# Kernel tuning notes

Measured on AMD Instinct MI355X. Metric: run time of the kernel, lower is better.

The kernel has to match this reference:

```python
import jax, jax.numpy as jnp
import numpy as np

EMBED_DIM = 1024
NUM_HEADS = 16
HEAD_DIM = EMBED_DIM // NUM_HEADS


def setup_inputs() -> dict:
    key = jax.random.key(0)
    k_x, k_wqkv, k_bqkv, k_wo, k_bo = jax.random.split(key, 5)
    B, T, C = 4, 2048, EMBED_DIM
    s_in = 1.0 / np.sqrt(C)
    return {
        "x": jax.random.normal(k_x, (B, T, C), dtype=jnp.float32),
        # torch Linear: weight [out,in]; we store transposed [in,out] for x @ W
        "w_qkv": jax.random.uniform(k_wqkv, (C, 3 * C), dtype=jnp.float32, minval=-s_in, maxval=s_in),
        "b_qkv": jax.random.uniform(k_bqkv, (3 * C,), dtype=jnp.float32, minval=-s_in, maxval=s_in),
        "w_out": jax.random.uniform(k_wo, (C, C), dtype=jnp.float32, minval=-s_in, maxval=s_in),
        "b_out": jax.random.uniform(k_bo, (C,), dtype=jnp.float32, minval=-s_in, maxval=s_in),
    }


def reference(x, w_qkv, b_qkv, w_out, b_out):
    B, T, C = x.shape
    H, D = NUM_HEADS, HEAD_DIM
    qkv = x @ w_qkv + b_qkv                       # [B,T,3C]
    qkv = qkv.reshape(B, T, 3, H, D)
    q, k, v = qkv[:, :, 0], qkv[:, :, 1], qkv[:, :, 2]   # [B,T,H,D]
    q = q.transpose(0, 2, 1, 3)                   # [B,H,T,D]
    k = k.transpose(0, 2, 1, 3)
    v = v.transpose(0, 2, 1, 3)
    scale = 1.0 / np.sqrt(D).astype(np.float32)
    att = jnp.einsum("bhqd,bhkd->bhqk", q, k) * scale   # [B,H,T,T]
    causal = jnp.tril(jnp.ones((T, T), dtype=bool))
    att = jnp.where(causal[None, None], att, -jnp.inf)
    att = jax.nn.softmax(att, axis=-1)
    y = jnp.einsum("bhqk,bhkd->bhqd", att, v)     # [B,H,T,D]
    y = y.transpose(0, 2, 1, 3).reshape(B, T, C)
    return y @ w_out + b_out
```

## Files before the change

### kernel.cpp

```cpp
#include <hip/hip_runtime.h>
#include <hip/hip_bf16.h>

#define EMBED 1024
#define NHEAD 16
#define HDIM  64
#define BATCH 4
#define SEQ   2048
#define BT    (BATCH*SEQ)
#define NQKV  (3*EMBED)

using bf16x8 = __attribute__((ext_vector_type(8))) short;
using f32x4  = __attribute__((ext_vector_type(4))) float;

__device__ __forceinline__ unsigned short f2bf(float f){
  union { float f; unsigned u; } v; v.f = f;
  unsigned r = v.u + 0x7FFFu + ((v.u >> 16) & 1u);
  return (unsigned short)(r >> 16);
}

__device__ __forceinline__ float exp2_hw(float x){
  float r; asm("v_exp_f32 %0, %1" : "=v"(r) : "v"(x)); return r;
}
__device__ __forceinline__ unsigned cvtpk_bf16(float lo, float hi){
  unsigned r; asm("v_cvt_pk_bf16_f32 %0, %1, %2" : "=v"(r) : "v"(lo), "v"(hi));
  return r;
}

__device__ __forceinline__ void gload_lds16(const void* g, void* l){
  __builtin_amdgcn_global_load_lds(
      (const __attribute__((address_space(1))) void*)g,
      (__attribute__((address_space(3))) void*)l, 16, 0, 0);
}

__global__ __launch_bounds__(256) void cvt_f32_bf16_k(
    const float* __restrict__ in, unsigned short* __restrict__ out, int n)
{
  int i = (blockIdx.x * 256 + threadIdx.x) * 4;
  if (i >= n) return;
  float4 v = *(const float4*)&in[i];
  ushort4 o;
  o.x = f2bf(v.x); o.y = f2bf(v.y); o.z = f2bf(v.z); o.w = f2bf(v.w);
  *(ushort4*)&out[i] = o;
}

__global__ __launch_bounds__(256) void transpose_cvt_k(
    const float* __restrict__ in, unsigned short* __restrict__ out, int R, int C)
{
  __shared__ float tile[32][33];
  int tx = threadIdx.x, ty = threadIdx.y;
  int c0 = blockIdx.x * 32, r0 = blockIdx.y * 32;
#pragma unroll
  for (int j = ty; j < 32; j += 8)
    tile[j][tx] = in[(size_t)(r0 + j) * C + c0 + tx];
  __syncthreads();
#pragma unroll
  for (int j = ty; j < 32; j += 8)
    out[(size_t)(c0 + j) * R + r0 + tx] = f2bf(tile[tx][j]);
}

template<int EPI>
__global__ __launch_bounds__(256) void gemm_bt(
    const unsigned short* __restrict__ A,
    const unsigned short* __restrict__ Bt,
    const float* __restrict__ bias,
    unsigned short* __restrict__ qp,
    unsigned short* __restrict__ kp,
    unsigned short* __restrict__ vp,
    float* __restrict__ outp,
    int M, int N, int K)
{
  __shared__ unsigned short As[2][128 * 32];
  __shared__ unsigned short Bs[2][128 * 32];
  const int tid = threadIdx.x;
  const int w = tid >> 6, lane = tid & 63;
  const int lr = lane & 15, lg = lane >> 4;
  const int gy = gridDim.y;
  const int lin = (int)(blockIdx.y * gridDim.x + blockIdx.x);
  const int cpx = (int)(gridDim.x * gy) >> 3;
  const int wg = (lin & 7) * cpx + (lin >> 3);
  const int m0 = (wg / gy) * 128, n0 = (wg % gy) * 128;
  const int wm = (w >> 1) * 64, wn = (w & 1) * 64;
  f32x4 acc[4][4] = {};

  int goff[2], dst[2];
#pragma unroll
  for (int i = 0; i < 2; i++) {
    int f = (w * 2 + i) * 512 + lane * 8;
    goff[i] = (f >> 5) * K + (f & 31);
    dst[i] = f;
  }
  const unsigned short* pA = A + (size_t)m0 * K;
  const unsigned short* pB = Bt + (size_t)n0 * K;

  const int nkt = K >> 5;

#pragma unroll
  for (int i = 0; i < 2; i++) {
    gload_lds16(pA + goff[i], &As[0][dst[i]]);
    gload_lds16(pB + goff[i], &Bs[0][dst[i]]);
  }

  int cur = 0;
  for (int t = 0; t < nkt; t++) {
    if (t + 1 < nkt) {
      const int kt = (t + 1) << 5;
#pragma unroll
      for (int i = 0; i < 2; i++) {
        gload_lds16(pA + goff[i] + kt, &As[cur ^ 1][dst[i]]);
        gload_lds16(pB + goff[i] + kt, &Bs[cur ^ 1][dst[i]]);
      }
      asm volatile("s_waitcnt vmcnt(4)" ::: "memory");
    } else {
      asm volatile("s_waitcnt vmcnt(0)" ::: "memory");
    }
    __builtin_amdgcn_s_barrier();
    __builtin_amdgcn_sched_barrier(0);

    bf16x8 af[4], bv[4];
#pragma unroll
    for (int mi = 0; mi < 4; mi++)
      af[mi] = *(const bf16x8*)&As[cur][(wm + mi * 16 + lr) * 32 + lg * 8];
#pragma unroll
    for (int ni = 0; ni < 4; ni++)
      bv[ni] = *(const bf16x8*)&Bs[cur][(wn + ni * 16 + lr) * 32 + lg * 8];
    __builtin_amdgcn_s_setprio(1);
#pragma unroll
    for (int mi = 0; mi < 4; mi++)
#pragma unroll
      for (int ni = 0; ni < 4; ni++)
        acc[mi][ni] = __builtin_amdgcn_mfma_f32_16x16x32_bf16(af[mi], bv[ni], acc[mi][ni], 0, 0, 0);
    __builtin_amdgcn_s_setprio(0);

    asm volatile("s_waitcnt lgkmcnt(0)" ::: "memory");
    __builtin_amdgcn_s_barrier();
    cur ^= 1;
  }

#pragma unroll
  for (int mi = 0; mi < 4; mi++)
#pragma unroll
    for (int ni = 0; ni < 4; ni++) {
      const int rowb = m0 + wm + mi * 16 + lg * 4;
      const int colb = n0 + wn + ni * 16 + lr;
      const float bv_ = bias[colb];
      if (EPI == 0) {
        int s = colb >> 10, hh = (colb & 1023) >> 6, d = colb & 63;
        int b = rowb >> 11, t = rowb & 2047;
        if (s == 2) {
          ushort4 o4;
          o4.x = f2bf(acc[mi][ni][0] + bv_);
          o4.y = f2bf(acc[mi][ni][1] + bv_);
          o4.z = f2bf(acc[mi][ni][2] + bv_);
          o4.w = f2bf(acc[mi][ni][3] + bv_);
          *(ushort4*)&vp[((size_t)(b * NHEAD + hh) * HDIM + d) * SEQ + t] = o4;
        } else {
          unsigned short* dst_ = (s == 0) ? qp : kp;
          const float scl = (s == 0) ? 0.18033688f : 1.0f;
#pragma unroll
          for (int r = 0; r < 4; r++)
            dst_[((size_t)(b * NHEAD + hh) * SEQ + t + r) * HDIM + d] =
                f2bf((acc[mi][ni][r] + bv_) * scl);
        }
      } else {
#pragma unroll
        for (int r = 0; r < 4; r++)
          outp[(size_t)(rowb + r) * N + colb] = acc[mi][ni][r] + bv_;
      }
    }
}

__device__ __forceinline__ void softmax_frag(
    f32x4 (&s)[4], float& m, f32x4& su, f32x4 (&o)[4],
    unsigned short* psrow, int qrow, int kbase, bool needmask,
    int lg, int lr, int pswz)
{
  const float NEG = -1e30f;
  if (needmask) {
#pragma unroll
    for (int n = 0; n < 4; n++)
#pragma unroll
      for (int r = 0; r < 4; r++) {
        if (kbase + n * 16 + lg * 4 + r > qrow) s[n][r] = NEG;
      }
  }
  float t0 = fmaxf(fmaxf(s[0][0], s[0][1]), fmaxf(s[0][2], s[0][3]));
  float t1 = fmaxf(fmaxf(s[1][0], s[1][1]), fmaxf(s[1][2], s[1][3]));
  float t2 = fmaxf(fmaxf(s[2][0], s[2][1]), fmaxf(s[2][2], s[2][3]));
  float t3 = fmaxf(fmaxf(s[3][0], s[3][1]), fmaxf(s[3][2], s[3][3]));
  float pm = fmaxf(fmaxf(t0, t1), fmaxf(t2, t3));
  if (__any(pm > m + 8.f)) {
    pm = fmaxf(pm, __shfl_xor(pm, 16, 64));
    pm = fmaxf(pm, __shfl_xor(pm, 32, 64));
    float mn = fmaxf(m, pm);
    float fac = exp2_hw(m - mn);
    m = mn;
    float fr[4];
#pragma unroll
    for (int r = 0; r < 4; r++) fr[r] = __shfl(fac, lg * 4 + r, 64);
#pragma unroll
    for (int r = 0; r < 4; r++) su[r] *= fr[r];
#pragma unroll
    for (int n = 0; n < 4; n++)
#pragma unroll
      for (int r = 0; r < 4; r++) o[n][r] *= fr[r];
  }
#pragma unroll
  for (int n = 0; n < 4; n++) {
    float p0 = exp2_hw(s[n][0] - m);
    float p1 = exp2_hw(s[n][1] - m);
    float p2 = exp2_hw(s[n][2] - m);
    float p3 = exp2_hw(s[n][3] - m);
    uint2 pk;
    pk.x = cvtpk_bf16(p0, p1);
    pk.y = cvtpk_bf16(p2, p3);
    int E = (lr * 64 + n * 16 + lg * 4) ^ pswz;
    *(uint2*)&psrow[E] = pk;
  }
}

__global__ __launch_bounds__(256) void attn_k(
    const unsigned short* __restrict__ Q,
    const unsigned short* __restrict__ K,
    const unsigned short* __restrict__ Vt,
    unsigned short* __restrict__ Y)
{
  __shared__ unsigned short Ks[2][64 * 64];
  __shared__ unsigned short Vs[2][64 * 64];
  __shared__ unsigned short Ps[4][32 * 64];

  const int tid = threadIdx.x;
  const int w = tid >> 6, lane = tid & 63;
  const int lr = lane & 15, lg = lane >> 4;
  const int bh = blockIdx.y;
  const int b = bh >> 4, h = bh & 15;
  const size_t base = (size_t)bh * SEQ * HDIM;
  const float NEG = -1e30f;
  const int pswz = (lr & 7) << 3;

  bf16x8 ones;
#pragma unroll
  for (int e = 0; e < 8; e++) ones[e] = (short)0x3F80;

  const int f0 = w * 128 + lane, f1 = f0 + 64;
  const int r0_ = f0 >> 3, c0_ = ((f0 & 7) ^ (r0_ & 7)) * 8;
  const int r1_ = f1 >> 3, c1_ = ((f1 & 7) ^ (r1_ & 7)) * 8;

  for (int seg = 0; seg < 2; seg++) {
    const int qb = seg ? (int)blockIdx.x : (15 - (int)blockIdx.x);
    const int qw0 = qb * 128 + w * 32;
    const int nk = 2 * qb + 2;

    bf16x8 aq[2][2];
#pragma unroll
    for (int f = 0; f < 2; f++)
#pragma unroll
      for (int kk = 0; kk < 2; kk++)
        aq[f][kk] = *(const bf16x8*)
            &Q[base + (size_t)(qw0 + f * 16 + lr) * HDIM + kk * 32 + lg * 8];

    f32x4 o0[4] = {}, o1[4] = {};
    f32x4 su0 = {}, su1 = {};
    float m0 = NEG, m1 = NEG;

    {
      const unsigned short* kxp = K + base;
      const unsigned short* vxp = Vt + base;
      gload_lds16(kxp + r0_ * HDIM + c0_, &Ks[0][f0 * 8]);
      gload_lds16(kxp + r1_ * HDIM + c1_, &Ks[0][f1 * 8]);
      gload_lds16(vxp + (size_t)r0_ * SEQ + c0_, &Vs[0][f0 * 8]);
      gload_lds16(vxp + (size_t)r1_ * SEQ + c1_, &Vs[0][f1 * 8]);
    }
    __syncthreads();

    int cur = 0;
    for (int kb = 0; kb < nk; kb++) {
      if (kb + 1 < nk) {
        const unsigned short* kxp = K + base + (size_t)(kb + 1) * 64 * HDIM;
        const unsigned short* vxp = Vt + base + (kb + 1) * 64;
        gload_lds16(kxp + r0_ * HDIM + c0_, &Ks[cur ^ 1][f0 * 8]);
        gload_lds16(kxp + r1_ * HDIM + c1_, &Ks[cur ^ 1][f1 * 8]);
        gload_lds16(vxp + (size_t)r0_ * SEQ + c0_, &Vs[cur ^ 1][f0 * 8]);
        gload_lds16(vxp + (size_t)r1_ * SEQ + c1_, &Vs[cur ^ 1][f1 * 8]);
      }

      const bool active = (kb * 64 <= qw0 + 31);
      if (active) {
        f32x4 s0[4] = {}, s1[4] = {};
        __builtin_amdgcn_s_setprio(1);
#pragma unroll
        for (int kk = 0; kk < 2; kk++) {
          bf16x8 bk[4];
#pragma unroll
          for (int n = 0; n < 4; n++) {
            int E = (n * 16 + lr) * 64 + kk * 32 + lg * 8;
            bk[n] = *(const bf16x8*)&Ks[cur][E ^ pswz];
          }
#pragma unroll
          for (int n = 0; n < 4; n++) {
            s0[n] = __builtin_amdgcn_mfma_f32_16x16x32_bf16(bk[n], aq[0][kk], s0[n], 0, 0, 0);
            s1[n] = __builtin_amdgcn_mfma_f32_16x16x32_bf16(bk[n], aq[1][kk], s1[n], 0, 0, 0);
          }
        }
        __builtin_amdgcn_s_setprio(0);

        const int kbase = kb * 64;
        softmax_frag(s0, m0, su0, o0, &Ps[w][0],
                     qw0 + lr, kbase, kbase + 63 > qw0, lg, lr, pswz);
        softmax_frag(s1, m1, su1, o1, &Ps[w][16 * 64],
                     qw0 + 16 + lr, kbase, kbase + 63 > qw0 + 16, lg, lr, pswz);

        __builtin_amdgcn_s_setprio(1);
#pragma unroll
        for (int kc = 0; kc < 2; kc++) {
          bf16x8 ap0 = *(const bf16x8*)&Ps[w][(lr * 64 + kc * 32 + lg * 8) ^ pswz];
          bf16x8 ap1 = *(const bf16x8*)&Ps[w][((16 + lr) * 64 + kc * 32 + lg * 8) ^ pswz];
          su0 = __builtin_amdgcn_mfma_f32_16x16x32_bf16(ap0, ones, su0, 0, 0, 0);
          su1 = __builtin_amdgcn_mfma_f32_16x16x32_bf16(ap1, ones, su1, 0, 0, 0);
#pragma unroll
          for (int n = 0; n < 4; n++) {
            int E = (n * 16 + lr) * 64 + kc * 32 + lg * 8;
            bf16x8 bv = *(const bf16x8*)&Vs[cur][E ^ pswz];
            o0[n] = __builtin_amdgcn_mfma_f32_16x16x32_bf16(ap0, bv, o0[n], 0, 0, 0);
            o1[n] = __builtin_amdgcn_mfma_f32_16x16x32_bf16(ap1, bv, o1[n], 0, 0, 0);
          }
        }
        __builtin_amdgcn_s_setprio(0);
      }

      __syncthreads();
      cur ^= 1;
    }

    float inv0[4], inv1[4];
#pragma unroll
    for (int r = 0; r < 4; r++) { inv0[r] = 1.f / su0[r]; inv1[r] = 1.f / su1[r]; }
#pragma unroll
    for (int n = 0; n < 4; n++)
#pragma unroll
      for (int r = 0; r < 4; r++) {
        int col = h * HDIM + n * 16 + lr;
        int t0 = qw0 + lg * 4 + r;
        Y[((size_t)(b * SEQ + t0)) * EMBED + col] = f2bf(o0[n][r] * inv0[r]);
        int t1 = qw0 + 16 + lg * 4 + r;
        Y[((size_t)(b * SEQ + t1)) * EMBED + col] = f2bf(o1[n][r] * inv1[r]);
      }
  }
}

extern "C" void kernel_launch(void* const* d_in, const int* in_sizes, int n_in,
                              void* d_out, int out_size, void* d_ws, size_t ws_size,
                              hipStream_t stream) {
  const float* x     = (const float*)d_in[0];
  const float* w_qkv = (const float*)d_in[1];
  const float* b_qkv = (const float*)d_in[2];
  const float* w_out = (const float*)d_in[3];
  const float* b_out = (const float*)d_in[4];
  float* outp = (float*)d_out;

  char* ws = (char*)d_ws;
  unsigned short* xb    = (unsigned short*)ws; ws += (size_t)BT * EMBED * 2;
  unsigned short* wqkvT = (unsigned short*)ws; ws += (size_t)NQKV * EMBED * 2;
  unsigned short* woutT = (unsigned short*)ws; ws += (size_t)EMBED * EMBED * 2;
  unsigned short* Qb    = (unsigned short*)ws; ws += (size_t)BATCH * NHEAD * SEQ * HDIM * 2;
  unsigned short* Kb    = (unsigned short*)ws; ws += (size_t)BATCH * NHEAD * SEQ * HDIM * 2;
  unsigned short* Vb    = (unsigned short*)ws; ws += (size_t)BATCH * NHEAD * SEQ * HDIM * 2;
  unsigned short* Yb    = (unsigned short*)ws; ws += (size_t)BT * EMBED * 2;

  cvt_f32_bf16_k<<<(BT * EMBED) / 1024, 256, 0, stream>>>(x, xb, BT * EMBED);
  transpose_cvt_k<<<dim3(NQKV / 32, EMBED / 32), dim3(32, 8), 0, stream>>>(w_qkv, wqkvT, EMBED, NQKV);
  transpose_cvt_k<<<dim3(EMBED / 32, EMBED / 32), dim3(32, 8), 0, stream>>>(w_out, woutT, EMBED, EMBED);

  gemm_bt<0><<<dim3(BT / 128, NQKV / 128), 256, 0, stream>>>(
      xb, wqkvT, b_qkv, Qb, Kb, Vb, nullptr, BT, NQKV, EMBED);

  attn_k<<<dim3(8, BATCH * NHEAD), 256, 0, stream>>>(Qb, Kb, Vb, Yb);

  gemm_bt<1><<<dim3(BT / 128, EMBED / 128), 256, 0, stream>>>(
      Yb, woutT, b_out, nullptr, nullptr, nullptr, outp, BT, EMBED, EMBED);
}
```

Before: 188.8 us.

## Split causal attention KV range across blocks with partial-softmax combine kernel

Attention now runs on twice as many blocks: each block handles two half-KV-range segments (first half of query block bx and second half of query block 15-bx), writing unnormalized fp32 partial outputs plus row max and sum to workspace. A new combine kernel merges the two partials per query block and writes bf16 Y. KV tiles shrink to 32 keys with new LDS swizzles, and the full syncthreads is replaced by explicit vmcnt/lgkmcnt waits plus raw barriers. This is meant to improve load balance and occupancy across CUs. The cost is an extra launch and fp32 partial traffic of about 32 MB written and read back.

```diff
diff --git a/kernel.cpp b/kernel.cpp
--- a/kernel.cpp
+++ b/kernel.cpp
@@ -169,15 +169,15 @@
     }
 }
 
-__device__ __forceinline__ void softmax_frag(
-    f32x4 (&s)[4], float& m, f32x4& su, f32x4 (&o)[4],
-    unsigned short* psrow, int qrow, int kbase, bool needmask,
-    int lg, int lr, int pswz)
+__device__ __forceinline__ void softmax_frag32(
+    f32x4 (&s)[2], float& m, f32x4& su, f32x4 (&o)[4],
+    unsigned short* psfrag, int qrow, int kbase, bool needmask,
+    int lg, int lr)
 {
   const float NEG = -1e30f;
   if (needmask) {
 #pragma unroll
-    for (int n = 0; n < 4; n++)
+    for (int n = 0; n < 2; n++)
 #pragma unroll
       for (int r = 0; r < 4; r++) {
         if (kbase + n * 16 + lg * 4 + r > qrow) s[n][r] = NEG;
@@ -185,9 +185,7 @@
   }
   float t0 = fmaxf(fmaxf(s[0][0], s[0][1]), fmaxf(s[0][2], s[0][3]));
   float t1 = fmaxf(fmaxf(s[1][0], s[1][1]), fmaxf(s[1][2], s[1][3]));
-  float t2 = fmaxf(fmaxf(s[2][0], s[2][1]), fmaxf(s[2][2], s[2][3]));
-  float t3 = fmaxf(fmaxf(s[3][0], s[3][1]), fmaxf(s[3][2], s[3][3]));
-  float pm = fmaxf(fmaxf(t0, t1), fmaxf(t2, t3));
+  float pm = fmaxf(t0, t1);
   if (__any(pm > m + 8.f)) {
     pm = fmaxf(pm, __shfl_xor(pm, 16, 64));
     pm = fmaxf(pm, __shfl_xor(pm, 32, 64));
@@ -205,7 +203,7 @@
       for (int r = 0; r < 4; r++) o[n][r] *= fr[r];
   }
 #pragma unroll
-  for (int n = 0; n < 4; n++) {
+  for (int n = 0; n < 2; n++) {
     float p0 = exp2_hw(s[n][0] - m);
     float p1 = exp2_hw(s[n][1] - m);
     float p2 = exp2_hw(s[n][2] - m);
@@ -213,8 +211,8 @@
     uint2 pk;
     pk.x = cvtpk_bf16(p0, p1);
     pk.y = cvtpk_bf16(p2, p3);
-    int E = (lr * 64 + n * 16 + lg * 4) ^ pswz;
-    *(uint2*)&psrow[E] = pk;
+    int E = lr * 32 + ((((2 * n) + (lg >> 1)) ^ (lr & 3)) << 3) + ((lg & 1) << 2);
+    *(uint2*)&psfrag[E] = pk;
   }
 }
 
@@ -222,17 +220,18 @@
     const unsigned short* __restrict__ Q,
     const unsigned short* __restrict__ K,
     const unsigned short* __restrict__ Vt,
-    unsigned short* __restrict__ Y)
-{
-  __shared__ unsigned short Ks[2][64 * 64];
-  __shared__ unsigned short Vs[2][64 * 64];
-  __shared__ unsigned short Ps[4][32 * 64];
+    float* __restrict__ Opart,
+    float* __restrict__ Mpart,
+    float* __restrict__ Spart)
+{
+  __shared__ unsigned short Ks[2][32 * 64];
+  __shared__ unsigned short Vs[2][64 * 32];
+  __shared__ unsigned short Ps[4][2 * 16 * 32];
 
   const int tid = threadIdx.x;
   const int w = tid >> 6, lane = tid & 63;
   const int lr = lane & 15, lg = lane >> 4;
-  const int bh = blockIdx.y;
-  const int b = bh >> 4, h = bh & 15;
+  const int bx = blockIdx.x, bh = blockIdx.y;
   const size_t base = (size_t)bh * SEQ * HDIM;
   const float NEG = -1e30f;
   const int pswz = (lr & 7) << 3;
@@ -241,14 +240,14 @@
 #pragma unroll
   for (int e = 0; e < 8; e++) ones[e] = (short)0x3F80;
 
-  const int f0 = w * 128 + lane, f1 = f0 + 64;
-  const int r0_ = f0 >> 3, c0_ = ((f0 & 7) ^ (r0_ & 7)) * 8;
-  const int r1_ = f1 >> 3, c1_ = ((f1 & 7) ^ (r1_ & 7)) * 8;
+  const int krow = tid >> 3, ksc = ((tid & 7) ^ (krow & 7)) * 8;
+  const int vrow = tid >> 2, vsc = ((tid & 3) ^ (vrow & 3)) * 8;
 
   for (int seg = 0; seg < 2; seg++) {
-    const int qb = seg ? (int)blockIdx.x : (15 - (int)blockIdx.x);
+    const int qb = seg ? (15 - bx) : bx;
+    const int k0 = seg ? (2 * qb + 2) : 0;
+    const int k1 = seg ? (4 * qb + 4) : (2 * qb + 2);
     const int qw0 = qb * 128 + w * 32;
-    const int nk = 2 * qb + 2;
 
     bf16x8 aq[2][2];
 #pragma unroll
@@ -262,64 +261,61 @@
     f32x4 su0 = {}, su1 = {};
     float m0 = NEG, m1 = NEG;
 
-    {
-      const unsigned short* kxp = K + base;
-      const unsigned short* vxp = Vt + base;
-      gload_lds16(kxp + r0_ * HDIM + c0_, &Ks[0][f0 * 8]);
-      gload_lds16(kxp + r1_ * HDIM + c1_, &Ks[0][f1 * 8]);
-      gload_lds16(vxp + (size_t)r0_ * SEQ + c0_, &Vs[0][f0 * 8]);
-      gload_lds16(vxp + (size_t)r1_ * SEQ + c1_, &Vs[0][f1 * 8]);
-    }
+    gload_lds16(K  + base + (size_t)(k0 * 32 + krow) * HDIM + ksc, &Ks[0][tid * 8]);
+    gload_lds16(Vt + base + (size_t)vrow * SEQ + k0 * 32 + vsc,    &Vs[0][tid * 8]);
     __syncthreads();
 
     int cur = 0;
-    for (int kb = 0; kb < nk; kb++) {
-      if (kb + 1 < nk) {
-        const unsigned short* kxp = K + base + (size_t)(kb + 1) * 64 * HDIM;
-        const unsigned short* vxp = Vt + base + (kb + 1) * 64;
-        gload_lds16(kxp + r0_ * HDIM + c0_, &Ks[cur ^ 1][f0 * 8]);
-        gload_lds16(kxp + r1_ * HDIM + c1_, &Ks[cur ^ 1][f1 * 8]);
-        gload_lds16(vxp + (size_t)r0_ * SEQ + c0_, &Vs[cur ^ 1][f0 * 8]);
-        gload_lds16(vxp + (size_t)r1_ * SEQ + c1_, &Vs[cur ^ 1][f1 * 8]);
-      }
-
-      const bool active = (kb * 64 <= qw0 + 31);
+    for (int kb = k0; kb < k1; kb++) {
+      if (kb + 1 < k1) {
+        gload_lds16(K  + base + (size_t)((kb + 1) * 32 + krow) * HDIM + ksc,
+                    &Ks[cur ^ 1][tid * 8]);
+        gload_lds16(Vt + base + (size_t)vrow * SEQ + (kb + 1) * 32 + vsc,
+                    &Vs[cur ^ 1][tid * 8]);
+        asm volatile("s_waitcnt vmcnt(2)" ::: "memory");
+      } else {
+        asm volatile("s_waitcnt vmcnt(0)" ::: "memory");
+      }
+      __builtin_amdgcn_s_barrier();
+      __builtin_amdgcn_sched_barrier(0);
+
+      const bool active = (kb * 32 <= qw0 + 31);
       if (active) {
-        f32x4 s0[4] = {}, s1[4] = {};
+        f32x4 s0[2] = {}, s1[2] = {};
         __builtin_amdgcn_s_setprio(1);
 #pragma unroll
         for (int kk = 0; kk < 2; kk++) {
-          bf16x8 bk[4];
-#pragma unroll
-          for (int n = 0; n < 4; n++) {
+          bf16x8 bk[2];
+#pragma unroll
+          for (int n = 0; n < 2; n++) {
             int E = (n * 16 + lr) * 64 + kk * 32 + lg * 8;
             bk[n] = *(const bf16x8*)&Ks[cur][E ^ pswz];
           }
 #pragma unroll
-          for (int n = 0; n < 4; n++) {
+          for (int n = 0; n < 2; n++) {
             s0[n] = __builtin_amdgcn_mfma_f32_16x16x32_bf16(bk[n], aq[0][kk], s0[n], 0, 0, 0);
             s1[n] = __builtin_amdgcn_mfma_f32_16x16x32_bf16(bk[n], aq[1][kk], s1[n], 0, 0, 0);
           }
         }
         __builtin_amdgcn_s_setprio(0);
 
-        const int kbase = kb * 64;
-        softmax_frag(s0, m0, su0, o0, &Ps[w][0],
-                     qw0 + lr, kbase, kbase + 63 > qw0, lg, lr, pswz);
-        softmax_frag(s1, m1, su1, o1, &Ps[w][16 * 64],
-                     qw0 + 16 + lr, kbase, kbase + 63 > qw0 + 16, lg, lr, pswz);
+        const int kbase = kb * 32;
+        softmax_frag32(s0, m0, su0, o0, &Ps[w][0],
+                       qw0 + lr, kbase, kbase + 31 > qw0, lg, lr);
+        softmax_frag32(s1, m1, su1, o1, &Ps[w][512],
+                       qw0 + 16 + lr, kbase, kbase + 31 > qw0 + 16, lg, lr);
 
         __builtin_amdgcn_s_setprio(1);
-#pragma unroll
-        for (int kc = 0; kc < 2; kc++) {
-          bf16x8 ap0 = *(const bf16x8*)&Ps[w][(lr * 64 + kc * 32 + lg * 8) ^ pswz];
-          bf16x8 ap1 = *(const bf16x8*)&Ps[w][((16 + lr) * 64 + kc * 32 + lg * 8) ^ pswz];
+        {
+          int Ea = lr * 32 + ((lg ^ (lr & 3)) << 3);
+          bf16x8 ap0 = *(const bf16x8*)&Ps[w][Ea];
+          bf16x8 ap1 = *(const bf16x8*)&Ps[w][512 + Ea];
           su0 = __builtin_amdgcn_mfma_f32_16x16x32_bf16(ap0, ones, su0, 0, 0, 0);
           su1 = __builtin_amdgcn_mfma_f32_16x16x32_bf16(ap1, ones, su1, 0, 0, 0);
 #pragma unroll
           for (int n = 0; n < 4; n++) {
-            int E = (n * 16 + lr) * 64 + kc * 32 + lg * 8;
-            bf16x8 bv = *(const bf16x8*)&Vs[cur][E ^ pswz];
+            int Ev = (n * 16 + lr) * 32 + ((lg ^ (lr & 3)) << 3);
+            bf16x8 bv = *(const bf16x8*)&Vs[cur][Ev];
             o0[n] = __builtin_amdgcn_mfma_f32_16x16x32_bf16(ap0, bv, o0[n], 0, 0, 0);
             o1[n] = __builtin_amdgcn_mfma_f32_16x16x32_bf16(ap1, bv, o1[n], 0, 0, 0);
           }
@@ -327,23 +323,64 @@
         __builtin_amdgcn_s_setprio(0);
       }
 
-      __syncthreads();
+      asm volatile("s_waitcnt lgkmcnt(0)" ::: "memory");
+      __builtin_amdgcn_s_barrier();
       cur ^= 1;
     }
 
-    float inv0[4], inv1[4];
-#pragma unroll
-    for (int r = 0; r < 4; r++) { inv0[r] = 1.f / su0[r]; inv1[r] = 1.f / su1[r]; }
+    const size_t pb = ((size_t)(bh * 16 + qb) * 2 + seg);
+    float* Op = Opart + pb * (128 * 64);
 #pragma unroll
     for (int n = 0; n < 4; n++)
 #pragma unroll
       for (int r = 0; r < 4; r++) {
-        int col = h * HDIM + n * 16 + lr;
-        int t0 = qw0 + lg * 4 + r;
-        Y[((size_t)(b * SEQ + t0)) * EMBED + col] = f2bf(o0[n][r] * inv0[r]);
-        int t1 = qw0 + 16 + lg * 4 + r;
-        Y[((size_t)(b * SEQ + t1)) * EMBED + col] = f2bf(o1[n][r] * inv1[r]);
-      }
+        Op[(w * 32 + lg * 4 + r) * 64 + n * 16 + lr] = o0[n][r];
+        Op[(w * 32 + 16 + lg * 4 + r) * 64 + n * 16 + lr] = o1[n][r];
+      }
+    if (lr == 0) {
+#pragma unroll
+      for (int r = 0; r < 4; r++) {
+        Spart[pb * 128 + w * 32 + lg * 4 + r] = su0[r];
+        Spart[pb * 128 + w * 32 + 16 + lg * 4 + r] = su1[r];
+      }
+    }
+    if (lg == 0) {
+      Mpart[pb * 128 + w * 32 + lr] = m0;
+      Mpart[pb * 128 + w * 32 + 16 + lr] = m1;
+    }
+  }
+}
+
+__global__ __launch_bounds__(256) void combine_k(
+    const float* __restrict__ Opart,
+    const float* __restrict__ Mpart,
+    const float* __restrict__ Spart,
+    unsigned short* __restrict__ Y)
+{
+  const int qb = blockIdx.x, bh = blockIdx.y;
+  const int b = bh >> 4, h = bh & 15;
+  const int tid = threadIdx.x;
+  const int row = tid >> 1, hc = (tid & 1) * 32;
+  const size_t p0 = ((size_t)(bh * 16 + qb) * 2);
+  const size_t p1 = p0 + 1;
+  const float m0 = Mpart[p0 * 128 + row], m1 = Mpart[p1 * 128 + row];
+  const float s0 = Spart[p0 * 128 + row], s1 = Spart[p1 * 128 + row];
+  const float ms = fmaxf(m0, m1);
+  const float w0 = exp2_hw(m0 - ms), w1 = exp2_hw(m1 - ms);
+  const float inv = 1.f / (s0 * w0 + s1 * w1);
+  const float* o0 = Opart + p0 * 8192 + row * 64 + hc;
+  const float* o1 = Opart + p1 * 8192 + row * 64 + hc;
+  unsigned short* y = Y + ((size_t)(b * SEQ) + qb * 128 + row) * EMBED + h * 64 + hc;
+#pragma unroll
+  for (int c = 0; c < 32; c += 4) {
+    float4 a = *(const float4*)&o0[c];
+    float4 d = *(const float4*)&o1[c];
+    ushort4 ov;
+    ov.x = f2bf((a.x * w0 + d.x * w1) * inv);
+    ov.y = f2bf((a.y * w0 + d.y * w1) * inv);
+    ov.z = f2bf((a.z * w0 + d.z * w1) * inv);
+    ov.w = f2bf((a.w * w0 + d.w * w1) * inv);
+    *(ushort4*)&y[c] = ov;
   }
 }
 
@@ -365,6 +402,9 @@
   unsigned short* Kb    = (unsigned short*)ws; ws += (size_t)BATCH * NHEAD * SEQ * HDIM * 2;
   unsigned short* Vb    = (unsigned short*)ws; ws += (size_t)BATCH * NHEAD * SEQ * HDIM * 2;
   unsigned short* Yb    = (unsigned short*)ws; ws += (size_t)BT * EMBED * 2;
+  float* Opart = (float*)ws; ws += (size_t)64 * 16 * 2 * 128 * 64 * 4;
+  float* Mpart = (float*)ws; ws += (size_t)64 * 16 * 2 * 128 * 4;
+  float* Spart = (float*)ws; ws += (size_t)64 * 16 * 2 * 128 * 4;
 
   cvt_f32_bf16_k<<<(BT * EMBED) / 1024, 256, 0, stream>>>(x, xb, BT * EMBED);
   transpose_cvt_k<<<dim3(NQKV / 32, EMBED / 32), dim3(32, 8), 0, stream>>>(w_qkv, wqkvT, EMBED, NQKV);
@@ -373,7 +413,8 @@
   gemm_bt<0><<<dim3(BT / 128, NQKV / 128), 256, 0, stream>>>(
       xb, wqkvT, b_qkv, Qb, Kb, Vb, nullptr, BT, NQKV, EMBED);
 
-  attn_k<<<dim3(8, BATCH * NHEAD), 256, 0, stream>>>(Qb, Kb, Vb, Yb);
+  attn_k<<<dim3(16, BATCH * NHEAD), 256, 0, stream>>>(Qb, Kb, Vb, Opart, Mpart, Spart);
+  combine_k<<<dim3(16, BATCH * NHEAD), 256, 0, stream>>>(Opart, Mpart, Spart, Yb);
 
   gemm_bt<1><<<dim3(BT / 128, EMBED / 128), 256, 0, stream>>>(
       Yb, woutT, b_out, nullptr, nullptr, nullptr, outp, BT, EMBED, EMBED);
```

Measured after the change: 230.0 us. 21.8% more time.

## Split attention work across 8 waves with 16 query rows each

Applied to the files above, without the earlier changes.

The attention kernel moves from 4 waves handling 32 query rows each to 8 waves (512 threads) handling 16 rows each, keeping the 128-row query block per workgroup. Each thread now issues one K and one V async load per tile instead of two, and the per-wave P scratch shrinks accordingly. The aim is more waves in flight to hide LDS and global latency, and causal masking that skips work at 16-row granularity. In exchange, each K/V tile read from LDS is reused by fewer rows per wave, so LDS read traffic per MFMA doubles, and there are more waves per barrier.

```diff
diff --git a/kernel.cpp b/kernel.cpp
--- a/kernel.cpp
+++ b/kernel.cpp
@@ -218,7 +218,7 @@
   }
 }
 
-__global__ __launch_bounds__(256) void attn_k(
+__global__ __launch_bounds__(512) void attn_k(
     const unsigned short* __restrict__ Q,
     const unsigned short* __restrict__ K,
     const unsigned short* __restrict__ Vt,
@@ -226,7 +226,7 @@
 {
   __shared__ unsigned short Ks[2][64 * 64];
   __shared__ unsigned short Vs[2][64 * 64];
-  __shared__ unsigned short Ps[4][32 * 64];
+  __shared__ unsigned short Ps[8][16 * 64];
 
   const int tid = threadIdx.x;
   const int w = tid >> 6, lane = tid & 63;
@@ -241,51 +241,39 @@
 #pragma unroll
   for (int e = 0; e < 8; e++) ones[e] = (short)0x3F80;
 
-  const int f0 = w * 128 + lane, f1 = f0 + 64;
-  const int r0_ = f0 >> 3, c0_ = ((f0 & 7) ^ (r0_ & 7)) * 8;
-  const int r1_ = f1 >> 3, c1_ = ((f1 & 7) ^ (r1_ & 7)) * 8;
+  const int r0_ = tid >> 3, c0_ = ((tid & 7) ^ (r0_ & 7)) * 8;
 
   for (int seg = 0; seg < 2; seg++) {
     const int qb = seg ? (int)blockIdx.x : (15 - (int)blockIdx.x);
-    const int qw0 = qb * 128 + w * 32;
+    const int qw0 = qb * 128 + w * 16;
     const int nk = 2 * qb + 2;
 
-    bf16x8 aq[2][2];
-#pragma unroll
-    for (int f = 0; f < 2; f++)
-#pragma unroll
-      for (int kk = 0; kk < 2; kk++)
-        aq[f][kk] = *(const bf16x8*)
-            &Q[base + (size_t)(qw0 + f * 16 + lr) * HDIM + kk * 32 + lg * 8];
-
-    f32x4 o0[4] = {}, o1[4] = {};
-    f32x4 su0 = {}, su1 = {};
-    float m0 = NEG, m1 = NEG;
-
-    {
-      const unsigned short* kxp = K + base;
-      const unsigned short* vxp = Vt + base;
-      gload_lds16(kxp + r0_ * HDIM + c0_, &Ks[0][f0 * 8]);
-      gload_lds16(kxp + r1_ * HDIM + c1_, &Ks[0][f1 * 8]);
-      gload_lds16(vxp + (size_t)r0_ * SEQ + c0_, &Vs[0][f0 * 8]);
-      gload_lds16(vxp + (size_t)r1_ * SEQ + c1_, &Vs[0][f1 * 8]);
-    }
+    bf16x8 aq[2];
+#pragma unroll
+    for (int kk = 0; kk < 2; kk++)
+      aq[kk] = *(const bf16x8*)
+          &Q[base + (size_t)(qw0 + lr) * HDIM + kk * 32 + lg * 8];
+
+    f32x4 o[4] = {};
+    f32x4 su = {};
+    float m = NEG;
+
+    gload_lds16(K  + base + (size_t)r0_ * HDIM + c0_, &Ks[0][tid * 8]);
+    gload_lds16(Vt + base + (size_t)r0_ * SEQ  + c0_, &Vs[0][tid * 8]);
     __syncthreads();
 
     int cur = 0;
     for (int kb = 0; kb < nk; kb++) {
       if (kb + 1 < nk) {
-        const unsigned short* kxp = K + base + (size_t)(kb + 1) * 64 * HDIM;
-        const unsigned short* vxp = Vt + base + (kb + 1) * 64;
-        gload_lds16(kxp + r0_ * HDIM + c0_, &Ks[cur ^ 1][f0 * 8]);
-        gload_lds16(kxp + r1_ * HDIM + c1_, &Ks[cur ^ 1][f1 * 8]);
-        gload_lds16(vxp + (size_t)r0_ * SEQ + c0_, &Vs[cur ^ 1][f0 * 8]);
-        gload_lds16(vxp + (size_t)r1_ * SEQ + c1_, &Vs[cur ^ 1][f1 * 8]);
-      }
-
-      const bool active = (kb * 64 <= qw0 + 31);
+        gload_lds16(K  + base + (size_t)((kb + 1) * 64 + r0_) * HDIM + c0_,
+                    &Ks[cur ^ 1][tid * 8]);
+        gload_lds16(Vt + base + (size_t)r0_ * SEQ + (kb + 1) * 64 + c0_,
+                    &Vs[cur ^ 1][tid * 8]);
+      }
+
+      const bool active = (kb * 64 <= qw0 + 15);
       if (active) {
-        f32x4 s0[4] = {}, s1[4] = {};
+        f32x4 s[4] = {};
         __builtin_amdgcn_s_setprio(1);
 #pragma unroll
         for (int kk = 0; kk < 2; kk++) {
@@ -296,53 +284,44 @@
             bk[n] = *(const bf16x8*)&Ks[cur][E ^ pswz];
           }
 #pragma unroll
+          for (int n = 0; n < 4; n++)
+            s[n] = __builtin_amdgcn_mfma_f32_16x16x32_bf16(bk[n], aq[kk], s[n], 0, 0, 0);
+        }
+        __builtin_amdgcn_s_setprio(0);
+
+        const int kbase = kb * 64;
+        softmax_frag(s, m, su, o, &Ps[w][0],
+                     qw0 + lr, kbase, kbase + 63 > qw0, lg, lr, pswz);
+
+        __builtin_amdgcn_s_setprio(1);
+#pragma unroll
+        for (int kc = 0; kc < 2; kc++) {
+          bf16x8 ap = *(const bf16x8*)&Ps[w][(lr * 64 + kc * 32 + lg * 8) ^ pswz];
+          su = __builtin_amdgcn_mfma_f32_16x16x32_bf16(ap, ones, su, 0, 0, 0);
+#pragma unroll
           for (int n = 0; n < 4; n++) {
-            s0[n] = __builtin_amdgcn_mfma_f32_16x16x32_bf16(bk[n], aq[0][kk], s0[n], 0, 0, 0);
-            s1[n] = __builtin_amdgcn_mfma_f32_16x16x32_bf16(bk[n], aq[1][kk], s1[n], 0, 0, 0);
+            int E = (n * 16 + lr) * 64 + kc * 32 + lg * 8;
+            bf16x8 bv = *(const bf16x8*)&Vs[cur][E ^ pswz];
+            o[n] = __builtin_amdgcn_mfma_f32_16x16x32_bf16(ap, bv, o[n], 0, 0, 0);
           }
         }
         __builtin_amdgcn_s_setprio(0);
-
-        const int kbase = kb * 64;
-        softmax_frag(s0, m0, su0, o0, &Ps[w][0],
-                     qw0 + lr, kbase, kbase + 63 > qw0, lg, lr, pswz);
-        softmax_frag(s1, m1, su1, o1, &Ps[w][16 * 64],
-                     qw0 + 16 + lr, kbase, kbase + 63 > qw0 + 16, lg, lr, pswz);
-
-        __builtin_amdgcn_s_setprio(1);
-#pragma unroll
-        for (int kc = 0; kc < 2; kc++) {
-          bf16x8 ap0 = *(const bf16x8*)&Ps[w][(lr * 64 + kc * 32 + lg * 8) ^ pswz];
-          bf16x8 ap1 = *(const bf16x8*)&Ps[w][((16 + lr) * 64 + kc * 32 + lg * 8) ^ pswz];
-          su0 = __builtin_amdgcn_mfma_f32_16x16x32_bf16(ap0, ones, su0, 0, 0, 0);
-          su1 = __builtin_amdgcn_mfma_f32_16x16x32_bf16(ap1, ones, su1, 0, 0, 0);
-#pragma unroll
-          for (int n = 0; n < 4; n++) {
-            int E = (n * 16 + lr) * 64 + kc * 32 + lg * 8;
-            bf16x8 bv = *(const bf16x8*)&Vs[cur][E ^ pswz];
-            o0[n] = __builtin_amdgcn_mfma_f32_16x16x32_bf16(ap0, bv, o0[n], 0, 0, 0);
-            o1[n] = __builtin_amdgcn_mfma_f32_16x16x32_bf16(ap1, bv, o1[n], 0, 0, 0);
-          }
-        }
-        __builtin_amdgcn_s_setprio(0);
       }
 
       __syncthreads();
       cur ^= 1;
     }
 
-    float inv0[4], inv1[4];
-#pragma unroll
-    for (int r = 0; r < 4; r++) { inv0[r] = 1.f / su0[r]; inv1[r] = 1.f / su1[r]; }
+    float inv[4];
+#pragma unroll
+    for (int r = 0; r < 4; r++) inv[r] = 1.f / su[r];
 #pragma unroll
     for (int n = 0; n < 4; n++)
 #pragma unroll
       for (int r = 0; r < 4; r++) {
         int col = h * HDIM + n * 16 + lr;
         int t0 = qw0 + lg * 4 + r;
-        Y[((size_t)(b * SEQ + t0)) * EMBED + col] = f2bf(o0[n][r] * inv0[r]);
-        int t1 = qw0 + 16 + lg * 4 + r;
-        Y[((size_t)(b * SEQ + t1)) * EMBED + col] = f2bf(o1[n][r] * inv1[r]);
+        Y[((size_t)(b * SEQ + t0)) * EMBED + col] = f2bf(o[n][r] * inv[r]);
       }
   }
 }
@@ -373,7 +352,7 @@
   gemm_bt<0><<<dim3(BT / 128, NQKV / 128), 256, 0, stream>>>(
       xb, wqkvT, b_qkv, Qb, Kb, Vb, nullptr, BT, NQKV, EMBED);
 
-  attn_k<<<dim3(8, BATCH * NHEAD), 256, 0, stream>>>(Qb, Kb, Vb, Yb);
+  attn_k<<<dim3(8, BATCH * NHEAD), 512, 0, stream>>>(Qb, Kb, Vb, Yb);
 
   gemm_bt<1><<<dim3(BT / 128, EMBED / 128), 256, 0, stream>>>(
       Yb, woutT, b_out, nullptr, nullptr, nullptr, outp, BT, EMBED, EMBED);
```

Result: faster. 175.0 us (median of 2 runs) (-7.3%).
